# Optimization experiments

Measured on AMD Instinct MI355X. Metric: run time of the kernel, lower is better.

## Reference

```python
import jax, jax.numpy as jnp
import numpy as np

N_NODES = 100000
N_HEDGES = 20000
N_PAIRS = 1600000
D = 128


def setup_inputs() -> dict:
    key = jax.random.key(0)
    k1, k2, k3, k4, k5 = jax.random.split(key, 5)
    features = jax.random.normal(k1, (N_NODES, D), dtype=jnp.float32)
    W = jax.random.normal(k2, (D, D), dtype=jnp.float32) * (1.0 / np.sqrt(D))
    b = jax.random.normal(k3, (D,), dtype=jnp.float32) * 0.01
    node_idx = jax.random.randint(k4, (N_PAIRS,), 0, N_NODES, dtype=jnp.int32)
    hedge_idx = jax.random.randint(k5, (N_PAIRS,), 0, N_HEDGES, dtype=jnp.int32)
    return {"features": features, "W": W, "b": b,
            "node_idx": node_idx, "hedge_idx": hedge_idx, "n_hedges": N_HEDGES}


def reference(features, W, b, node_idx, hedge_idx, n_hedges):
    # features: [N, D]; (node_idx, hedge_idx): [E] incidence pairs
    N = features.shape[0]
    ones = jnp.ones(node_idx.shape, dtype=features.dtype)
    # node -> hyperedge mean (DGL copy_u + mean over 'in' etype)
    deg_e = jax.ops.segment_sum(ones, hedge_idx, num_segments=n_hedges)  # [He]
    h_edge = jax.ops.segment_sum(features[node_idx], hedge_idx, num_segments=n_hedges)
    h_edge = h_edge / jnp.maximum(deg_e, 1.0)[:, None]  # zero-degree edges -> 0
    # hyperedge -> node mean (copy_u + mean over 'contains' etype)
    deg_n = jax.ops.segment_sum(ones, node_idx, num_segments=N)  # [N]
    h_node = jax.ops.segment_sum(h_edge[hedge_idx], node_idx, num_segments=N)
    h_node = h_node / jnp.maximum(deg_n, 1.0)[:, None]
    # nn.Linear: x @ W.T + b
    return h_node @ W.T + b
```

## Files before the change

kernel.cpp:

```cpp
#include <hip/hip_runtime.h>

static constexpr int kD = 128;
static constexpr int kHedges = 20000;

static constexpr int kNCE = 157;
static constexpr int kCapCE = 11264;
static constexpr int kNCN = 196;
static constexpr int kCapCN = 9216;
static constexpr int kSliceE4 = 1664;
static constexpr int kSliceN4 = 1408;
static constexpr int kPmax = 3200;
static constexpr int kNBmax = 196;

typedef __attribute__((ext_vector_type(8))) short bf16x8;
typedef __attribute__((ext_vector_type(4))) float f32x4;

__device__ __forceinline__ float u2f(unsigned u) { return __uint_as_float(u); }
__device__ __forceinline__ unsigned f2u(float f) { return __float_as_uint(f); }

__device__ __forceinline__ unsigned bfpack(float x, float y) {
  unsigned ux = f2u(x); ux = (ux + 0x7FFFu + ((ux >> 16) & 1u)) >> 16;
  unsigned uy = f2u(y); uy = (uy + 0x7FFFu + ((uy >> 16) & 1u)) & 0xFFFF0000u;
  return ux | uy;
}
__device__ __forceinline__ void bf8_acc(uint4 v, float* a) {
  a[0] += u2f(v.x << 16); a[1] += u2f(v.x & 0xFFFF0000u);
  a[2] += u2f(v.y << 16); a[3] += u2f(v.y & 0xFFFF0000u);
  a[4] += u2f(v.z << 16); a[5] += u2f(v.z & 0xFFFF0000u);
  a[6] += u2f(v.w << 16); a[7] += u2f(v.w & 0xFFFF0000u);
}

__global__ __launch_bounds__(512) void partition_coarse(
    const float* __restrict__ feat, unsigned* __restrict__ feat_bf, int n_feat,
    const float* __restrict__ W, unsigned* __restrict__ Wbf,
    const int* __restrict__ node_idx, const int* __restrict__ hedge_idx,
    int n_pairs, int pgrid,
    int* __restrict__ gcnt_e, int* __restrict__ buf_e,
    int* __restrict__ gcnt_n, int* __restrict__ buf_n) {
  __shared__ unsigned lraw[kPmax];
  __shared__ unsigned lbuf[kPmax];
  __shared__ int hist[kNBmax], gshift[kNBmax];
  __shared__ int wtot[8];
  const int tid = threadIdx.x;
  {
    const int n8 = n_feat >> 3;
    for (int t = blockIdx.x * 512 + tid; t < n8; t += gridDim.x * 512) {
      long long i = (long long)t * 8;
      const float4 v0 = *(const float4*)(feat + i);
      const float4 v1 = *(const float4*)(feat + i + 4);
      uint4 o;
      o.x = bfpack(v0.x, v0.y); o.y = bfpack(v0.z, v0.w);
      o.z = bfpack(v1.x, v1.y); o.w = bfpack(v1.z, v1.w);
      *(uint4*)(feat_bf + (i >> 1)) = o;
    }
  }
  for (int t = blockIdx.x * 512 + tid; t < kD * 64; t += gridDim.x * 512) {
    int row = t >> 6, m = t & 63;
    Wbf[t] = bfpack(W[row * kD + 2 * m], W[row * kD + 2 * m + 1]);
  }
  const bool isEdge = (blockIdx.x < pgrid);
  const int cchunk = isEdge ? blockIdx.x : blockIdx.x - pgrid;
  const int per_block = (n_pairs + pgrid - 1) / pgrid;
  const int s = cchunk * per_block;
  const int e = min(s + per_block, n_pairs);
  const int cnt = max(e - s, 0);
  const int nb      = isEdge ? kNCE : kNCN;
  const int shift   = isEdge ? 7 : 9;
  const int pshift  = isEdge ? 15 : 17;
  const int* __restrict__ kidx = isEdge ? hedge_idx : node_idx;
  const int* __restrict__ pidx = isEdge ? node_idx : hedge_idx;
  int* __restrict__ gcnt = isEdge ? gcnt_e : gcnt_n;
  int* __restrict__ bufo = isEdge ? buf_e : buf_n;
  const long long capc = isEdge ? kCapCE : kCapCN;
  const unsigned kmask = (1u << pshift) - 1u;
  const int lowmask = (1 << shift) - 1;

  for (int i = tid; i < nb; i += 512) hist[i] = 0;
  __syncthreads();
  for (int i = s + tid; i < e; i += 512) {
    const unsigned k = (unsigned)kidx[i];
    const unsigned p = (unsigned)pidx[i];
    lraw[i - s] = (p << pshift) | k;
    atomicAdd(&hist[k >> shift], 1);
  }
  __syncthreads();
  {
    const int lane = tid & 63, wid = tid >> 6;
    int v = (tid < nb) ? hist[tid] : 0;
    int x = v;
#pragma unroll
    for (int d = 1; d < 64; d <<= 1) {
      int y = __shfl_up(x, d, 64);
      if (lane >= d) x += y;
    }
    if (lane == 63) wtot[wid] = x;
    __syncthreads();
    int add = 0;
    for (int w = 0; w < wid; ++w) add += wtot[w];
    if (tid < nb) {
      int lofs = x + add - v;
      int base = (v > 0) ? atomicAdd(&gcnt[tid], v) : 0;
      gshift[tid] = base - lofs;
      hist[tid] = lofs;
    }
  }
  __syncthreads();
  for (int i = tid; i < cnt; i += 512) {
    const unsigned v = lraw[i];
    const int b = (int)((v & kmask) >> shift);
    const int pos = atomicAdd(&hist[b], 1);
    lbuf[pos] = v;
  }
  __syncthreads();
  for (int i = tid; i < cnt; i += 512) {
    const unsigned v = lbuf[i];
    const int k = (int)(v & kmask);
    const int p = (int)(v >> pshift);
    const int b = k >> shift;
    const int pe = gshift[b] + i;
    if (pe < capc) bufo[(long long)b * capc + pe] = (p << shift) | (k & lowmask);
  }
}

__global__ __launch_bounds__(1024) void subsort_kernel(
    int* __restrict__ buf_e, const int* __restrict__ gcnt_e, int* __restrict__ seg_e,
    int* __restrict__ buf_n, const int* __restrict__ gcnt_n, int* __restrict__ seg_n) {
  __shared__ int sbuf[kCapCE];
  __shared__ int bins[513];
  __shared__ int cur[512];
  __shared__ int segs[513];
  __shared__ int wtot[16];
  const int tid = threadIdx.x;
  int nbins, shift, cnt; int* src; int* segout;
  if (blockIdx.x < kNCE) {
    int cb = blockIdx.x; nbins = 128; shift = 7;
    src = buf_e + (long long)cb * kCapCE;
    cnt = min(gcnt_e[cb], kCapCE);
    segout = seg_e + cb * 129;
  } else {
    int cb = blockIdx.x - kNCE; nbins = 512; shift = 9;
    src = buf_n + (long long)cb * kCapCN;
    cnt = min(gcnt_n[cb], kCapCN);
    segout = seg_n + cb * 513;
  }
  const int mask = nbins - 1;
  for (int i = tid; i < nbins; i += 1024) bins[i] = 0;
  __syncthreads();
  for (int i = tid; i < cnt; i += 1024) atomicAdd(&bins[src[i] & mask], 1);
  __syncthreads();
  const int lane = tid & 63, wid = tid >> 6;
  int v = (tid < nbins) ? bins[tid] : 0;
  int x = v;
#pragma unroll
  for (int d = 1; d < 64; d <<= 1) {
    int y = __shfl_up(x, d, 64);
    if (lane >= d) x += y;
  }
  if (lane == 63) wtot[wid] = x;
  __syncthreads();
  int add = 0;
  for (int w = 0; w < wid; ++w) add += wtot[w];
  if (tid < nbins) { segs[tid + 1] = x + add; cur[tid] = x + add - v; }
  if (tid == 0) segs[0] = 0;
  __syncthreads();
  for (int i = tid; i < cnt; i += 1024) {
    int p = src[i];
    int r = atomicAdd(&cur[p & mask], 1);
    sbuf[r] = p >> shift;
  }
  __syncthreads();
  for (int i = tid; i < cnt; i += 1024) src[i] = sbuf[i];
  for (int j = tid; j <= nbins; j += 1024) segout[j] = segs[j];
}

__global__ __launch_bounds__(256) void gather_edge_fused(
    const unsigned* __restrict__ feat_bf, const int* __restrict__ buf_e,
    const int* __restrict__ seg_e, const unsigned* __restrict__ Wbf,
    unsigned* __restrict__ t_edge, int n_hedges) {
  __shared__ int ebuf[kSliceE4];
  __shared__ int segl[17];
  __shared__ unsigned hbf[16][68];
  __shared__ float hout[16][132];
  const int b = blockIdx.x;
  const int tid = threadIdx.x;
  const int h0 = b * 16;
  const int cb = h0 >> 7, j0 = h0 & 127;
  if (tid < 17) segl[tid] = seg_e[cb * 129 + j0 + tid];
  __syncthreads();
  const int sbase = segl[0];
  const int n_sl = min(segl[16] - sbase, kSliceE4);
  const int* src = buf_e + (long long)cb * kCapCE + sbase;
  for (int i = tid; i < n_sl; i += 256) ebuf[i] = src[i];
  __syncthreads();
  const int g = tid >> 4, lane = tid & 15, cw = lane * 4;
  const int gh = h0 + g;
  float a[8] = {}, a2[8] = {};
  int deg = 0;
  if (gh < n_hedges) {
    deg = segl[g + 1] - segl[g];
    const int s0 = min(segl[g] - sbase, n_sl);
    const int e0 = min(segl[g + 1] - sbase, n_sl);
    int j = s0;
    const int jend8 = s0 + ((e0 - s0) & ~7);
    if (j < jend8) {
      uint4 A0 = *(const uint4*)(feat_bf + (long long)ebuf[j] * 64 + cw);
      uint4 A1 = *(const uint4*)(feat_bf + (long long)ebuf[j + 1] * 64 + cw);
      uint4 A2 = *(const uint4*)(feat_bf + (long long)ebuf[j + 2] * 64 + cw);
      uint4 A3 = *(const uint4*)(feat_bf + (long long)ebuf[j + 3] * 64 + cw);
      uint4 A4 = *(const uint4*)(feat_bf + (long long)ebuf[j + 4] * 64 + cw);
      uint4 A5 = *(const uint4*)(feat_bf + (long long)ebuf[j + 5] * 64 + cw);
      uint4 A6 = *(const uint4*)(feat_bf + (long long)ebuf[j + 6] * 64 + cw);
      uint4 A7 = *(const uint4*)(feat_bf + (long long)ebuf[j + 7] * 64 + cw);
      j += 8;
      for (; j < jend8; j += 8) {
        uint4 B0 = *(const uint4*)(feat_bf + (long long)ebuf[j] * 64 + cw);
        uint4 B1 = *(const uint4*)(feat_bf + (long long)ebuf[j + 1] * 64 + cw);
        uint4 B2 = *(const uint4*)(feat_bf + (long long)ebuf[j + 2] * 64 + cw);
        uint4 B3 = *(const uint4*)(feat_bf + (long long)ebuf[j + 3] * 64 + cw);
        uint4 B4 = *(const uint4*)(feat_bf + (long long)ebuf[j + 4] * 64 + cw);
        uint4 B5 = *(const uint4*)(feat_bf + (long long)ebuf[j + 5] * 64 + cw);
        uint4 B6 = *(const uint4*)(feat_bf + (long long)ebuf[j + 6] * 64 + cw);
        uint4 B7 = *(const uint4*)(feat_bf + (long long)ebuf[j + 7] * 64 + cw);
        bf8_acc(A0, a); bf8_acc(A1, a2); bf8_acc(A2, a); bf8_acc(A3, a2);
        bf8_acc(A4, a); bf8_acc(A5, a2); bf8_acc(A6, a); bf8_acc(A7, a2);
        A0 = B0; A1 = B1; A2 = B2; A3 = B3;
        A4 = B4; A5 = B5; A6 = B6; A7 = B7;
      }
      bf8_acc(A0, a); bf8_acc(A1, a2); bf8_acc(A2, a); bf8_acc(A3, a2);
      bf8_acc(A4, a); bf8_acc(A5, a2); bf8_acc(A6, a); bf8_acc(A7, a2);
    }
    for (; j < e0; ++j) {
      uint4 v = *(const uint4*)(feat_bf + (long long)ebuf[j] * 64 + cw);
      bf8_acc(v, a);
    }
  }
  {
    const float inv = 1.0f / fmaxf((float)deg, 1.0f);
    uint4 o;
    o.x = bfpack((a[0] + a2[0]) * inv, (a[1] + a2[1]) * inv);
    o.y = bfpack((a[2] + a2[2]) * inv, (a[3] + a2[3]) * inv);
    o.z = bfpack((a[4] + a2[4]) * inv, (a[5] + a2[5]) * inv);
    o.w = bfpack((a[6] + a2[6]) * inv, (a[7] + a2[7]) * inv);
    *(uint4*)(&hbf[g][cw]) = o;
  }
  __syncthreads();
  {
    const int wv = tid >> 6;
    const int l = tid & 63;
    const int frow = l & 15;
    const int kgrp = l >> 4;
    f32x4 acc0 = {0.f, 0.f, 0.f, 0.f}, acc1 = {0.f, 0.f, 0.f, 0.f};
#pragma unroll
    for (int kk = 0; kk < 4; ++kk) {
      const int wofs = kk * 16 + kgrp * 4;
      bf16x8 af = *(const bf16x8*)(&hbf[frow][wofs]);
      bf16x8 bf0 = *(const bf16x8*)(Wbf + ((2 * wv) * 16 + frow) * 64 + wofs);
      bf16x8 bf1 = *(const bf16x8*)(Wbf + ((2 * wv + 1) * 16 + frow) * 64 + wofs);
      acc0 = __builtin_amdgcn_mfma_f32_16x16x32_bf16(af, bf0, acc0, 0, 0, 0);
      acc1 = __builtin_amdgcn_mfma_f32_16x16x32_bf16(af, bf1, acc1, 0, 0, 0);
    }
#pragma unroll
    for (int r = 0; r < 4; ++r) {
      hout[kgrp * 4 + r][(2 * wv) * 16 + frow] = acc0[r];
      hout[kgrp * 4 + r][(2 * wv + 1) * 16 + frow] = acc1[r];
    }
  }
  __syncthreads();
  if (gh < n_hedges) {
    const float* hr = &hout[g][lane * 8];
    uint4 o;
    o.x = bfpack(hr[0], hr[1]);
    o.y = bfpack(hr[2], hr[3]);
    o.z = bfpack(hr[4], hr[5]);
    o.w = bfpack(hr[6], hr[7]);
    *(uint4*)(t_edge + (long long)gh * 64 + cw) = o;
  }
}

__global__ __launch_bounds__(256) void gather_node_v4(
    const unsigned* __restrict__ t_edge, const int* __restrict__ buf_n,
    const int* __restrict__ seg_n, const float* __restrict__ bias,
    float* __restrict__ out, int n_nodes) {
  __shared__ int ebuf[kSliceN4];
  __shared__ int segl[65];
  const int b = blockIdx.x;
  const int tid = threadIdx.x;
  const int n0 = b * 64;
  const int cb = n0 >> 9, j0 = n0 & 511;
  if (tid < 65) segl[tid] = seg_n[cb * 513 + j0 + tid];
  __syncthreads();
  const int sbase = segl[0];
  const int n_sl = min(segl[64] - sbase, kSliceN4);
  const int* src = buf_n + (long long)cb * kCapCN + sbase;
  for (int i = tid; i < n_sl; i += 256) ebuf[i] = src[i];
  __syncthreads();
  const int g = tid >> 4, lane = tid & 15, cw = lane * 4;
  const float4 b0 = *(const float4*)(bias + lane * 8);
  const float4 b1 = *(const float4*)(bias + lane * 8 + 4);
  for (int nl = g; nl < 64; nl += 16) {
    int gn = n0 + nl;
    if (gn >= n_nodes) continue;
    const int deg = segl[nl + 1] - segl[nl];
    const int s0 = min(segl[nl] - sbase, n_sl);
    const int e0 = min(segl[nl + 1] - sbase, n_sl);
    float a[8] = {}, a2[8] = {};
    int j = s0;
    const int jend8 = s0 + ((e0 - s0) & ~7);
    if (j < jend8) {
      uint4 A0 = *(const uint4*)(t_edge + (long long)ebuf[j] * 64 + cw);
      uint4 A1 = *(const uint4*)(t_edge + (long long)ebuf[j + 1] * 64 + cw);
      uint4 A2 = *(const uint4*)(t_edge + (long long)ebuf[j + 2] * 64 + cw);
      uint4 A3 = *(const uint4*)(t_edge + (long long)ebuf[j + 3] * 64 + cw);
      uint4 A4 = *(const uint4*)(t_edge + (long long)ebuf[j + 4] * 64 + cw);
      uint4 A5 = *(const uint4*)(t_edge + (long long)ebuf[j + 5] * 64 + cw);
      uint4 A6 = *(const uint4*)(t_edge + (long long)ebuf[j + 6] * 64 + cw);
      uint4 A7 = *(const uint4*)(t_edge + (long long)ebuf[j + 7] * 64 + cw);
      j += 8;
      for (; j < jend8; j += 8) {
        uint4 B0 = *(const uint4*)(t_edge + (long long)ebuf[j] * 64 + cw);
        uint4 B1 = *(const uint4*)(t_edge + (long long)ebuf[j + 1] * 64 + cw);
        uint4 B2 = *(const uint4*)(t_edge + (long long)ebuf[j + 2] * 64 + cw);
        uint4 B3 = *(const uint4*)(t_edge + (long long)ebuf[j + 3] * 64 + cw);
        uint4 B4 = *(const uint4*)(t_edge + (long long)ebuf[j + 4] * 64 + cw);
        uint4 B5 = *(const uint4*)(t_edge + (long long)ebuf[j + 5] * 64 + cw);
        uint4 B6 = *(const uint4*)(t_edge + (long long)ebuf[j + 6] * 64 + cw);
        uint4 B7 = *(const uint4*)(t_edge + (long long)ebuf[j + 7] * 64 + cw);
        bf8_acc(A0, a); bf8_acc(A1, a2); bf8_acc(A2, a); bf8_acc(A3, a2);
        bf8_acc(A4, a); bf8_acc(A5, a2); bf8_acc(A6, a); bf8_acc(A7, a2);
        A0 = B0; A1 = B1; A2 = B2; A3 = B3;
        A4 = B4; A5 = B5; A6 = B6; A7 = B7;
      }
      bf8_acc(A0, a); bf8_acc(A1, a2); bf8_acc(A2, a); bf8_acc(A3, a2);
      bf8_acc(A4, a); bf8_acc(A5, a2); bf8_acc(A6, a); bf8_acc(A7, a2);
    }
    for (; j < e0; ++j) {
      uint4 v = *(const uint4*)(t_edge + (long long)ebuf[j] * 64 + cw);
      bf8_acc(v, a);
    }
#pragma unroll
    for (int t = 0; t < 8; ++t) a[t] += a2[t];
    float inv = 1.0f / fmaxf((float)deg, 1.0f);
    float4 o0, o1;
    o0.x = fmaf(a[0], inv, b0.x); o0.y = fmaf(a[1], inv, b0.y);
    o0.z = fmaf(a[2], inv, b0.z); o0.w = fmaf(a[3], inv, b0.w);
    o1.x = fmaf(a[4], inv, b1.x); o1.y = fmaf(a[5], inv, b1.y);
    o1.z = fmaf(a[6], inv, b1.z); o1.w = fmaf(a[7], inv, b1.w);
    float* op = out + (long long)gn * kD + lane * 8;
    *(float4*)op = o0;
    *(float4*)(op + 4) = o1;
  }
}

extern "C" void kernel_launch(void* const* d_in, const int* in_sizes, int n_in,
                              void* d_out, int out_size, void* d_ws, size_t ws_size,
                              hipStream_t stream) {
  const float* feat      = (const float*)d_in[0];
  const float* W         = (const float*)d_in[1];
  const float* b         = (const float*)d_in[2];
  const int*   node_idx  = (const int*)d_in[3];
  const int*   hedge_idx = (const int*)d_in[4];

  const int n_pairs  = in_sizes[3];
  const int n_nodes  = in_sizes[0] / kD;
  const int n_hedges = kHedges;
  const int n_feat   = in_sizes[0];

  unsigned* feat_bf = (unsigned*)d_out;

  const int n_rows_pad = ((n_hedges + 63) / 64) * 64;
  unsigned* t_edge = (unsigned*)d_ws;
  int* buf_e = (int*)(t_edge + (size_t)n_rows_pad * 64);
  int* buf_n = buf_e + (size_t)kNCE * kCapCE;
  int* seg_e = buf_n + (size_t)kNCN * kCapCN;
  int* seg_n = seg_e + (size_t)kNCE * 129;
  int* gcnt_e = seg_n + (size_t)kNCN * 513;
  int* gcnt_n = gcnt_e + kNCE;
  unsigned* Wbf = (unsigned*)(gcnt_n + kNCN);

  hipMemsetAsync(gcnt_e, 0, (size_t)(kNCE + kNCN) * sizeof(int), stream);

  int pgrid = (n_pairs + kPmax - 1) / kPmax;
  if (pgrid < 512) pgrid = 512;

  partition_coarse<<<2 * pgrid, 512, 0, stream>>>(
      feat, feat_bf, n_feat, W, Wbf,
      node_idx, hedge_idx, n_pairs, pgrid, gcnt_e, buf_e, gcnt_n, buf_n);

  subsort_kernel<<<kNCE + kNCN, 1024, 0, stream>>>(
      buf_e, gcnt_e, seg_e, buf_n, gcnt_n, seg_n);

  gather_edge_fused<<<(n_hedges + 15) / 16, 256, 0, stream>>>(
      feat_bf, buf_e, seg_e, Wbf, t_edge, n_hedges);

  gather_node_v4<<<(n_nodes + 63) / 64, 256, 0, stream>>>(
      t_edge, buf_n, seg_n, b, (float*)d_out, n_nodes);
}
```

Measured before the change: 249.0 us.

## Fuse node-side subsort into node gather kernel via per-half-bucket LDS sort

The node-side counting sort moves out of the shared subsort kernel and into the node gather kernel. Each block takes half of a coarse node bucket (256 nodes), histograms and scatters the pair list into LDS, then gathers t_edge rows straight from LDS indices. This drops a global write/read round trip of the node buffer and the seg_n array, and leaves subsort handling only the edge side. In exchange, each coarse bucket's list is read twice (once per half block), grid parallelism shrinks to 392 blocks of 512 threads, and the larger LDS footprint may lower occupancy.

```diff
diff --git a/kernel.cpp b/kernel.cpp
--- a/kernel.cpp
+++ b/kernel.cpp
@@ -8,7 +8,7 @@
 static constexpr int kNCN = 196;
 static constexpr int kCapCN = 9216;
 static constexpr int kSliceE4 = 1664;
-static constexpr int kSliceN4 = 1408;
+static constexpr int kCapHN = 4608;
 static constexpr int kPmax = 3200;
 static constexpr int kNBmax = 196;
 
@@ -122,34 +122,24 @@
   }
 }
 
-__global__ __launch_bounds__(1024) void subsort_kernel(
-    int* __restrict__ buf_e, const int* __restrict__ gcnt_e, int* __restrict__ seg_e,
-    int* __restrict__ buf_n, const int* __restrict__ gcnt_n, int* __restrict__ seg_n) {
+__global__ __launch_bounds__(1024) void subsort_edge(
+    int* __restrict__ buf_e, const int* __restrict__ gcnt_e, int* __restrict__ seg_e) {
   __shared__ int sbuf[kCapCE];
-  __shared__ int bins[513];
-  __shared__ int cur[512];
-  __shared__ int segs[513];
+  __shared__ int bins[129];
+  __shared__ int cur[128];
+  __shared__ int segs[129];
   __shared__ int wtot[16];
   const int tid = threadIdx.x;
-  int nbins, shift, cnt; int* src; int* segout;
-  if (blockIdx.x < kNCE) {
-    int cb = blockIdx.x; nbins = 128; shift = 7;
-    src = buf_e + (long long)cb * kCapCE;
-    cnt = min(gcnt_e[cb], kCapCE);
-    segout = seg_e + cb * 129;
-  } else {
-    int cb = blockIdx.x - kNCE; nbins = 512; shift = 9;
-    src = buf_n + (long long)cb * kCapCN;
-    cnt = min(gcnt_n[cb], kCapCN);
-    segout = seg_n + cb * 513;
-  }
-  const int mask = nbins - 1;
-  for (int i = tid; i < nbins; i += 1024) bins[i] = 0;
-  __syncthreads();
-  for (int i = tid; i < cnt; i += 1024) atomicAdd(&bins[src[i] & mask], 1);
+  const int cb = blockIdx.x;
+  int* src = buf_e + (long long)cb * kCapCE;
+  const int cnt = min(gcnt_e[cb], kCapCE);
+  int* segout = seg_e + cb * 129;
+  if (tid < 128) bins[tid] = 0;
+  __syncthreads();
+  for (int i = tid; i < cnt; i += 1024) atomicAdd(&bins[src[i] & 127], 1);
   __syncthreads();
   const int lane = tid & 63, wid = tid >> 6;
-  int v = (tid < nbins) ? bins[tid] : 0;
+  int v = (tid < 128) ? bins[tid] : 0;
   int x = v;
 #pragma unroll
   for (int d = 1; d < 64; d <<= 1) {
@@ -160,17 +150,17 @@
   __syncthreads();
   int add = 0;
   for (int w = 0; w < wid; ++w) add += wtot[w];
-  if (tid < nbins) { segs[tid + 1] = x + add; cur[tid] = x + add - v; }
+  if (tid < 128) { segs[tid + 1] = x + add; cur[tid] = x + add - v; }
   if (tid == 0) segs[0] = 0;
   __syncthreads();
   for (int i = tid; i < cnt; i += 1024) {
     int p = src[i];
-    int r = atomicAdd(&cur[p & mask], 1);
-    sbuf[r] = p >> shift;
+    int r = atomicAdd(&cur[p & 127], 1);
+    sbuf[r] = p >> 7;
   }
   __syncthreads();
   for (int i = tid; i < cnt; i += 1024) src[i] = sbuf[i];
-  for (int j = tid; j <= nbins; j += 1024) segout[j] = segs[j];
+  if (tid <= 128) segout[tid] = segs[tid];
 }
 
 __global__ __launch_bounds__(256) void gather_edge_fused(
@@ -277,54 +267,84 @@
   }
 }
 
-__global__ __launch_bounds__(256) void gather_node_v4(
+__global__ __launch_bounds__(512) void gather_node_v5(
     const unsigned* __restrict__ t_edge, const int* __restrict__ buf_n,
-    const int* __restrict__ seg_n, const float* __restrict__ bias,
+    const int* __restrict__ gcnt_n, const float* __restrict__ bias,
     float* __restrict__ out, int n_nodes) {
-  __shared__ int ebuf[kSliceN4];
-  __shared__ int segl[65];
-  const int b = blockIdx.x;
+  __shared__ int sbuf[kCapHN];
+  __shared__ int bins[256];
+  __shared__ int cur[256];
+  __shared__ int segs[257];
+  __shared__ int wtot[8];
   const int tid = threadIdx.x;
-  const int n0 = b * 64;
-  const int cb = n0 >> 9, j0 = n0 & 511;
-  if (tid < 65) segl[tid] = seg_n[cb * 513 + j0 + tid];
-  __syncthreads();
-  const int sbase = segl[0];
-  const int n_sl = min(segl[64] - sbase, kSliceN4);
-  const int* src = buf_n + (long long)cb * kCapCN + sbase;
-  for (int i = tid; i < n_sl; i += 256) ebuf[i] = src[i];
+  const int cb = blockIdx.x >> 1, hf = blockIdx.x & 1;
+  const int* src = buf_n + (long long)cb * kCapCN;
+  const int cnt = min(gcnt_n[cb], kCapCN);
+  if (tid < 256) bins[tid] = 0;
+  __syncthreads();
+  for (int i = tid; i < cnt; i += 512) {
+    const unsigned v = (unsigned)src[i];
+    if (((v >> 8) & 1u) == (unsigned)hf) atomicAdd(&bins[v & 255u], 1);
+  }
+  __syncthreads();
+  {
+    const int lane = tid & 63, wid = tid >> 6;
+    int v = (tid < 256) ? bins[tid] : 0;
+    int x = v;
+#pragma unroll
+    for (int d = 1; d < 64; d <<= 1) {
+      int y = __shfl_up(x, d, 64);
+      if (lane >= d) x += y;
+    }
+    if (lane == 63) wtot[wid] = x;
+    __syncthreads();
+    int add = 0;
+    for (int w = 0; w < wid; ++w) add += wtot[w];
+    if (tid < 256) { segs[tid + 1] = x + add; cur[tid] = x + add - v; }
+    if (tid == 0) segs[0] = 0;
+  }
+  __syncthreads();
+  for (int i = tid; i < cnt; i += 512) {
+    const unsigned v = (unsigned)src[i];
+    if (((v >> 8) & 1u) == (unsigned)hf) {
+      int r = atomicAdd(&cur[v & 255u], 1);
+      if (r < kCapHN) sbuf[r] = (int)(v >> 9);
+    }
+  }
   __syncthreads();
   const int g = tid >> 4, lane = tid & 15, cw = lane * 4;
   const float4 b0 = *(const float4*)(bias + lane * 8);
   const float4 b1 = *(const float4*)(bias + lane * 8 + 4);
-  for (int nl = g; nl < 64; nl += 16) {
-    int gn = n0 + nl;
+  const int n_sl = min(segs[256], kCapHN);
+  const int nbase = cb * 512 + hf * 256;
+  for (int nl = g; nl < 256; nl += 32) {
+    int gn = nbase + nl;
     if (gn >= n_nodes) continue;
-    const int deg = segl[nl + 1] - segl[nl];
-    const int s0 = min(segl[nl] - sbase, n_sl);
-    const int e0 = min(segl[nl + 1] - sbase, n_sl);
+    const int deg = segs[nl + 1] - segs[nl];
+    const int s0 = min(segs[nl], n_sl);
+    const int e0 = min(segs[nl + 1], n_sl);
     float a[8] = {}, a2[8] = {};
     int j = s0;
     const int jend8 = s0 + ((e0 - s0) & ~7);
     if (j < jend8) {
-      uint4 A0 = *(const uint4*)(t_edge + (long long)ebuf[j] * 64 + cw);
-      uint4 A1 = *(const uint4*)(t_edge + (long long)ebuf[j + 1] * 64 + cw);
-      uint4 A2 = *(const uint4*)(t_edge + (long long)ebuf[j + 2] * 64 + cw);
-      uint4 A3 = *(const uint4*)(t_edge + (long long)ebuf[j + 3] * 64 + cw);
-      uint4 A4 = *(const uint4*)(t_edge + (long long)ebuf[j + 4] * 64 + cw);
-      uint4 A5 = *(const uint4*)(t_edge + (long long)ebuf[j + 5] * 64 + cw);
-      uint4 A6 = *(const uint4*)(t_edge + (long long)ebuf[j + 6] * 64 + cw);
-      uint4 A7 = *(const uint4*)(t_edge + (long long)ebuf[j + 7] * 64 + cw);
+      uint4 A0 = *(const uint4*)(t_edge + (long long)sbuf[j] * 64 + cw);
+      uint4 A1 = *(const uint4*)(t_edge + (long long)sbuf[j + 1] * 64 + cw);
+      uint4 A2 = *(const uint4*)(t_edge + (long long)sbuf[j + 2] * 64 + cw);
+      uint4 A3 = *(const uint4*)(t_edge + (long long)sbuf[j + 3] * 64 + cw);
+      uint4 A4 = *(const uint4*)(t_edge + (long long)sbuf[j + 4] * 64 + cw);
+      uint4 A5 = *(const uint4*)(t_edge + (long long)sbuf[j + 5] * 64 + cw);
+      uint4 A6 = *(const uint4*)(t_edge + (long long)sbuf[j + 6] * 64 + cw);
+      uint4 A7 = *(const uint4*)(t_edge + (long long)sbuf[j + 7] * 64 + cw);
       j += 8;
       for (; j < jend8; j += 8) {
-        uint4 B0 = *(const uint4*)(t_edge + (long long)ebuf[j] * 64 + cw);
-        uint4 B1 = *(const uint4*)(t_edge + (long long)ebuf[j + 1] * 64 + cw);
-        uint4 B2 = *(const uint4*)(t_edge + (long long)ebuf[j + 2] * 64 + cw);
-        uint4 B3 = *(const uint4*)(t_edge + (long long)ebuf[j + 3] * 64 + cw);
-        uint4 B4 = *(const uint4*)(t_edge + (long long)ebuf[j + 4] * 64 + cw);
-        uint4 B5 = *(const uint4*)(t_edge + (long long)ebuf[j + 5] * 64 + cw);
-        uint4 B6 = *(const uint4*)(t_edge + (long long)ebuf[j + 6] * 64 + cw);
-        uint4 B7 = *(const uint4*)(t_edge + (long long)ebuf[j + 7] * 64 + cw);
+        uint4 B0 = *(const uint4*)(t_edge + (long long)sbuf[j] * 64 + cw);
+        uint4 B1 = *(const uint4*)(t_edge + (long long)sbuf[j + 1] * 64 + cw);
+        uint4 B2 = *(const uint4*)(t_edge + (long long)sbuf[j + 2] * 64 + cw);
+        uint4 B3 = *(const uint4*)(t_edge + (long long)sbuf[j + 3] * 64 + cw);
+        uint4 B4 = *(const uint4*)(t_edge + (long long)sbuf[j + 4] * 64 + cw);
+        uint4 B5 = *(const uint4*)(t_edge + (long long)sbuf[j + 5] * 64 + cw);
+        uint4 B6 = *(const uint4*)(t_edge + (long long)sbuf[j + 6] * 64 + cw);
+        uint4 B7 = *(const uint4*)(t_edge + (long long)sbuf[j + 7] * 64 + cw);
         bf8_acc(A0, a); bf8_acc(A1, a2); bf8_acc(A2, a); bf8_acc(A3, a2);
         bf8_acc(A4, a); bf8_acc(A5, a2); bf8_acc(A6, a); bf8_acc(A7, a2);
         A0 = B0; A1 = B1; A2 = B2; A3 = B3;
@@ -334,7 +354,7 @@
       bf8_acc(A4, a); bf8_acc(A5, a2); bf8_acc(A6, a); bf8_acc(A7, a2);
     }
     for (; j < e0; ++j) {
-      uint4 v = *(const uint4*)(t_edge + (long long)ebuf[j] * 64 + cw);
+      uint4 v = *(const uint4*)(t_edge + (long long)sbuf[j] * 64 + cw);
       bf8_acc(v, a);
     }
 #pragma unroll
@@ -372,8 +392,7 @@
   int* buf_e = (int*)(t_edge + (size_t)n_rows_pad * 64);
   int* buf_n = buf_e + (size_t)kNCE * kCapCE;
   int* seg_e = buf_n + (size_t)kNCN * kCapCN;
-  int* seg_n = seg_e + (size_t)kNCE * 129;
-  int* gcnt_e = seg_n + (size_t)kNCN * 513;
+  int* gcnt_e = seg_e + (size_t)kNCE * 129;
   int* gcnt_n = gcnt_e + kNCE;
   unsigned* Wbf = (unsigned*)(gcnt_n + kNCN);
 
@@ -386,12 +405,11 @@
       feat, feat_bf, n_feat, W, Wbf,
       node_idx, hedge_idx, n_pairs, pgrid, gcnt_e, buf_e, gcnt_n, buf_n);
 
-  subsort_kernel<<<kNCE + kNCN, 1024, 0, stream>>>(
-      buf_e, gcnt_e, seg_e, buf_n, gcnt_n, seg_n);
+  subsort_edge<<<kNCE, 1024, 0, stream>>>(buf_e, gcnt_e, seg_e);
 
   gather_edge_fused<<<(n_hedges + 15) / 16, 256, 0, stream>>>(
       feat_bf, buf_e, seg_e, Wbf, t_edge, n_hedges);
 
-  gather_node_v4<<<(n_nodes + 63) / 64, 256, 0, stream>>>(
-      t_edge, buf_n, seg_n, b, (float*)d_out, n_nodes);
-}
+  gather_node_v5<<<2 * kNCN, 512, 0, stream>>>(
+      t_edge, buf_n, gcnt_n, b, (float*)d_out, n_nodes);
+}
```

New measurement: 258.7 us. 3.9% more time.
